# Optimization experiments

Measured on AMD Instinct MI355X. Metric: run time of the kernel, lower is better.

The kernel has to match this reference:

```python
import jax, jax.numpy as jnp
import numpy as np

MARGIN = 1.0
EPS = 1e-12


def setup_inputs() -> dict:
    key = jax.random.key(0)
    k1, k2, k3 = jax.random.split(key, 3)
    inputs = jax.random.normal(k1, (8192, 128), dtype=jnp.float32)
    targets = jax.random.randint(k2, (8192,), 0, 64, dtype=jnp.int64)
    center = jax.random.normal(k3, (16, 128), dtype=jnp.float32)
    return {"inputs": inputs, "targets": targets, "center": center}


def reference(inputs, targets, center):
    n = inputs.shape[0]
    # pairwise Euclidean distances via ||a||^2 + ||b||^2 - 2 a.b  (matches addmm_ trick)
    sq = jnp.sum(inputs * inputs, axis=1)                      # [n]
    dist2 = sq[:, None] + sq[None, :] - 2.0 * (inputs @ inputs.T)
    dist = jnp.sqrt(jnp.clip(dist2, EPS))                      # [n, n]

    mask = targets[:, None] == targets[None, :]                # same-class mask [n, n]

    # batch-hard mining, fully vectorized (replaces per-row python loops)
    dist_ap = jnp.max(jnp.where(mask, dist, -jnp.inf), axis=1)  # hardest positive
    neg_min = jnp.min(jnp.where(mask, jnp.inf, dist), axis=1)   # hardest negative
    has_neg = jnp.any(~mask, axis=1)
    dist_an = jnp.where(has_neg, neg_min, dist_ap + MARGIN)

    # center augmentation: min over distances to L2-normalized prototypes
    cn = center / jnp.linalg.norm(center, axis=1, keepdims=True)       # [P, d]
    dc = jnp.sqrt(jnp.sum((inputs[:, None, :] - cn[None, :, :]) ** 2, axis=-1))  # [n, P]
    dc = jnp.clip(dc, EPS)
    dist_an = jnp.minimum(dist_an, jnp.min(dc, axis=1))

    # MarginRankingLoss with y=1: mean(relu(dist_ap - dist_an + margin))
    loss = jnp.mean(jnp.maximum(dist_ap - dist_an + MARGIN, 0.0))
    return loss
```

## Files before the change

kernel.cpp:

```cpp
#include <hip/hip_runtime.h>


#define N_ROWS 8192
#define DIM 128
#define KDIM 192
#define ROWB 384
#define NPROTO 16
#define NSTRIP 16
#define MARGIN_F 1.0f
#define EPS_F 1e-12f
#define BIAS_F 32768.0f

typedef __attribute__((ext_vector_type(8))) short short8;
typedef __attribute__((ext_vector_type(4))) float float4v;
typedef __attribute__((ext_vector_type(4))) unsigned uint4v;

static __device__ __forceinline__ unsigned f2bf(float f) {
  unsigned u = __float_as_uint(f);
  u += 0x7fffu + ((u >> 16) & 1u);
  return u >> 16;
}

static __device__ __forceinline__ void gload_lds16(const void* g, void* l) {
  __builtin_amdgcn_global_load_lds(
      (const __attribute__((address_space(1))) unsigned*)g,
      (__attribute__((address_space(3))) unsigned*)l, 16, 0, 0);
}

__global__ void prep_kernel(const float* __restrict__ x,
                            const float* __restrict__ center,
                            const int* __restrict__ tgt,
                            char* __restrict__ xbf,
                            float* __restrict__ sq,
                            float* __restrict__ mindc,
                            float* __restrict__ out) {
  __shared__ float scn[NPROTO * DIM];
  int tid = threadIdx.x;
  if (blockIdx.x == 0 && tid == 0) out[0] = 0.0f;
  int rloc = tid >> 4, l = tid & 15;
  {
    float v[8];
    float ss = 0.f;
#pragma unroll
    for (int j = 0; j < 8; ++j) {
      v[j] = center[rloc * DIM + l * 8 + j];
      ss += v[j] * v[j];
    }
#pragma unroll
    for (int m = 1; m < 16; m <<= 1) ss += __shfl_xor(ss, m, 64);
    float inv = 1.0f / sqrtf(ss);
#pragma unroll
    for (int j = 0; j < 8; ++j) scn[rloc * DIM + l * 8 + j] = v[j] * inv;
  }
  __syncthreads();

  int row = blockIdx.x * 16 + rloc;
  float4 v0 = ((const float4*)x)[row * 32 + l * 2];
  float4 v1 = ((const float4*)x)[row * 32 + l * 2 + 1];
  float ss = v0.x * v0.x + v0.y * v0.y + v0.z * v0.z + v0.w * v0.w +
             v1.x * v1.x + v1.y * v1.y + v1.z * v1.z + v1.w * v1.w;
  float dots[NPROTO];
#pragma unroll
  for (int p = 0; p < NPROTO; ++p) {
    const float* c = &scn[p * DIM + l * 8];
    dots[p] = v0.x * c[0] + v0.y * c[1] + v0.z * c[2] + v0.w * c[3] +
              v1.x * c[4] + v1.y * c[5] + v1.z * c[6] + v1.w * c[7];
  }
#pragma unroll
  for (int m = 1; m < 16; m <<= 1) {
    ss += __shfl_xor(ss, m, 64);
#pragma unroll
    for (int p = 0; p < NPROTO; ++p) dots[p] += __shfl_xor(dots[p], m, 64);
  }
  uint4 pk;
  pk.x = f2bf(v0.x) | (f2bf(v0.y) << 16);
  pk.y = f2bf(v0.z) | (f2bf(v0.w) << 16);
  pk.z = f2bf(v1.x) | (f2bf(v1.y) << 16);
  pk.w = f2bf(v1.z) | (f2bf(v1.w) << 16);
  *(uint4*)(xbf + (size_t)row * ROWB + l * 16) = pk;
  int cls = tgt[row];
  if (l < 8) {
    unsigned wv = (cls & 1) ? 0xC3000000u : 0x0000C300u;
    uint4 oh;
    oh.x = ((cls >> 1) == (l * 4 + 0)) ? wv : 0u;
    oh.y = ((cls >> 1) == (l * 4 + 1)) ? wv : 0u;
    oh.z = ((cls >> 1) == (l * 4 + 2)) ? wv : 0u;
    oh.w = ((cls >> 1) == (l * 4 + 3)) ? wv : 0u;
    *(uint4*)(xbf + (size_t)row * ROWB + 256 + l * 16) = oh;
  }
  if (l == 0) {
    float mind2 = INFINITY;
#pragma unroll
    for (int p = 0; p < NPROTO; ++p)
      mind2 = fminf(mind2, ss + 1.0f - 2.0f * dots[p]);
    sq[row] = ss;
    mindc[row] = fmaxf(sqrtf(fmaxf(mind2, 0.0f)), EPS_F);
  }
}

__global__ __launch_bounds__(256, 1) void
pairdist_kernel(const char* __restrict__ xbf, const float* __restrict__ sq,
                float* __restrict__ pmax, float* __restrict__ pmin) {
  __shared__ __align__(16) char bl[3][24576];
  __shared__ __align__(16) float sqlds[512];
  const int wave = threadIdx.x >> 6, lane = threadIdx.x & 63;
  const int q = lane >> 4, l16 = lane & 15;
  const int rg = blockIdx.x >> 4, strip = blockIdx.x & 15;
  const int rowbase = rg * 256 + wave * 64;
  const int stripbase = strip * 512;

  const int slot = threadIdx.x;
  const char* const srcstrip = xbf + (size_t)stripbase * ROWB;
  int soff[6];
#pragma unroll
  for (int r = 0; r < 6; ++r) {
    int o = r * 4096 + slot * 16;
    int c = o / ROWB;
    soff[r] = c * ROWB + ((o - c * ROWB) ^ ((c & 7) << 4));
  }

  auto stage = [&](int s, char* buf) {
    const char* g = srcstrip + (size_t)s * 24576;
#pragma unroll
    for (int r = 0; r < 6; ++r)
      gload_lds16(g + soff[r], buf + r * 4096 + wave * 1024);
  };

  short8 a[4][6];
#pragma unroll
  for (int rt = 0; rt < 4; ++rt) {
    const char* ar = xbf + (size_t)(rowbase + rt * 16 + l16) * ROWB + q * 16;
#pragma unroll
    for (int kc = 0; kc < 6; ++kc) a[rt][kc] = *(const short8*)(ar + kc * 64);
#pragma unroll
    for (int kc = 4; kc < 6; ++kc) {
      uint4v u = __builtin_bit_cast(uint4v, a[rt][kc]);
      u ^= 0x80008000u;
      a[rt][kc] = __builtin_bit_cast(short8, u);
    }
  }
#pragma unroll
  for (int rt = 0; rt < 4; ++rt)
#pragma unroll
    for (int kc = 0; kc < 6; ++kc)
      asm volatile("" : "+v"(a[rt][kc]));

  if (wave < 2)
    gload_lds16((const char*)(sq + stripbase) + wave * 1024 + lane * 16,
                (char*)sqlds + wave * 1024 + lane * 16);
  stage(0, bl[0]);
  stage(1, bl[1]);

  int roffb[6];
#pragma unroll
  for (int kc = 0; kc < 6; ++kc)
    roffb[kc] = (l16 * ROWB + kc * 64 + q * 16) ^ ((l16 & 7) << 4);

  float maxp[16], minn[16];
#pragma unroll
  for (int i = 0; i < 16; ++i) { maxp[i] = -INFINITY; minn[i] = INFINITY; }

  asm volatile("s_waitcnt vmcnt(6)" ::: "memory");
  __builtin_amdgcn_s_barrier();
  asm volatile("" ::: "memory");

#pragma unroll 1
  for (int s = 0; s < 8; ++s) {
    if (s + 2 < 8) stage(s + 2, bl[(s + 2) % 3]);
    const char* cur = bl[s % 3];
#pragma unroll
    for (int p = 0; p < 4; ++p) {
      const char* bufp = cur + p * 6144;
      float sqc = sqlds[s * 64 + p * 16 + l16];
      short8 b[6];
#pragma unroll
      for (int kc = 0; kc < 6; ++kc)
        b[kc] = *(const short8*)(bufp + roffb[kc]);
      float4v acc[4];
#pragma unroll
      for (int rt = 0; rt < 4; ++rt) acc[rt] = (float4v){0.f, 0.f, 0.f, 0.f};
      __builtin_amdgcn_s_setprio(1);
#pragma unroll
      for (int kc = 0; kc < 6; ++kc)
#pragma unroll
        for (int rt = 0; rt < 4; ++rt)
          acc[rt] = __builtin_amdgcn_mfma_f32_16x16x32_bf16(a[rt][kc], b[kc],
                                                            acc[rt], 0, 0, 0);
      __builtin_amdgcn_s_setprio(0);
#pragma unroll
      for (int rt = 0; rt < 4; ++rt)
#pragma unroll
        for (int r = 0; r < 4; ++r) {
          float v = fmaf(-2.0f, acc[rt][r], sqc);
          int idx = rt * 4 + r;
          maxp[idx] = fmaxf(maxp[idx], v);
          minn[idx] = fminf(minn[idx], v);
        }
    }
    if (s < 7) {
      if (s + 2 < 8)
        asm volatile("s_waitcnt vmcnt(6)" ::: "memory");
      else
        asm volatile("s_waitcnt vmcnt(0)" ::: "memory");
      __builtin_amdgcn_s_barrier();
      asm volatile("" ::: "memory");
    }
  }

#pragma unroll
  for (int m = 1; m < 16; m <<= 1)
#pragma unroll
    for (int i = 0; i < 16; ++i) {
      maxp[i] = fmaxf(maxp[i], __shfl_xor(maxp[i], m, 64));
      minn[i] = fminf(minn[i], __shfl_xor(minn[i], m, 64));
    }
  if (l16 == 0) {
    float* pM = pmax + (size_t)strip * N_ROWS + rowbase + q * 4;
    float* pm = pmin + (size_t)strip * N_ROWS + rowbase + q * 4;
#pragma unroll
    for (int rt = 0; rt < 4; ++rt)
#pragma unroll
      for (int r = 0; r < 4; ++r) {
        pM[rt * 16 + r] = maxp[rt * 4 + r];
        pm[rt * 16 + r] = minn[rt * 4 + r];
      }
  }
}

__global__ void finalize_kernel(const float* __restrict__ pmax,
                                const float* __restrict__ pmin,
                                const float* __restrict__ sq,
                                const float* __restrict__ mindc,
                                float* __restrict__ out) {
  __shared__ float wsum[4];
  int i = blockIdx.x * 256 + threadIdx.x;
  float maxv = -INFINITY, minv = INFINITY;
#pragma unroll
  for (int s = 0; s < NSTRIP; ++s) {
    maxv = fmaxf(maxv, pmax[s * N_ROWS + i]);
    minv = fminf(minv, pmin[s * N_ROWS + i]);
  }
  float si = sq[i];
  float dap = sqrtf(fmaxf(si + (maxv - BIAS_F), EPS_F));
  float dan = (minv > 16384.0f) ? (dap + MARGIN_F)
                                : sqrtf(fmaxf(si + minv, EPS_F));
  dan = fminf(dan, mindc[i]);
  float c = fmaxf(dap - dan + MARGIN_F, 0.0f) * (1.0f / (float)N_ROWS);
#pragma unroll
  for (int m = 1; m < 64; m <<= 1) c += __shfl_xor(c, m, 64);
  int lane = threadIdx.x & 63, wv = threadIdx.x >> 6;
  if (lane == 0) wsum[wv] = c;
  __syncthreads();
  if (threadIdx.x == 0) atomicAdd(out, wsum[0] + wsum[1] + wsum[2] + wsum[3]);
}

extern "C" void kernel_launch(void* const* d_in, const int* in_sizes, int n_in,
                              void* d_out, int out_size, void* d_ws, size_t ws_size,
                              hipStream_t stream) {
  const float* inputs = (const float*)d_in[0];
  const int* targets = (const int*)d_in[1];
  const float* center = (const float*)d_in[2];
  char* ws = (char*)d_ws;
  char* xbf    = ws;
  float* sq    = (float*)(ws + 3145728);
  float* mindc = (float*)(ws + 3178496);
  float* pmax  = (float*)(ws + 3211264);
  float* pmin  = (float*)(ws + 3735552);
  float* out   = (float*)d_out;

  prep_kernel<<<512, 256, 0, stream>>>(inputs, center, targets, xbf, sq, mindc, out);
  pairdist_kernel<<<512, 256, 0, stream>>>(xbf, sq, pmax, pmin);
  finalize_kernel<<<32, 256, 0, stream>>>(pmax, pmin, sq, mindc, out);
}
```

Baseline: 104.6 us.

## Replace one-hot class bias in GEMM K-dim with explicit target-compare masking

The earlier version encoded class membership as extra one-hot K columns (K=192) with a large bias, so the MFMA produced a biased distance that separated positives from negatives. This change drops those columns, reducing K to 128, row bytes to 256, and LDS staging per stage. Same-class masking is now done per element by comparing targets, which are loaded into registers and LDS. It cuts MFMA work and memory traffic by a third and pays for it with extra compares and selects in the epilogue.

```diff
diff --git a/kernel.cpp b/kernel.cpp
--- a/kernel.cpp
+++ b/kernel.cpp
@@ -3,17 +3,14 @@
 
 #define N_ROWS 8192
 #define DIM 128
-#define KDIM 192
-#define ROWB 384
+#define ROWB 256
 #define NPROTO 16
 #define NSTRIP 16
 #define MARGIN_F 1.0f
 #define EPS_F 1e-12f
-#define BIAS_F 32768.0f
 
 typedef __attribute__((ext_vector_type(8))) short short8;
 typedef __attribute__((ext_vector_type(4))) float float4v;
-typedef __attribute__((ext_vector_type(4))) unsigned uint4v;
 
 static __device__ __forceinline__ unsigned f2bf(float f) {
   unsigned u = __float_as_uint(f);
@@ -29,7 +26,6 @@
 
 __global__ void prep_kernel(const float* __restrict__ x,
                             const float* __restrict__ center,
-                            const int* __restrict__ tgt,
                             char* __restrict__ xbf,
                             float* __restrict__ sq,
                             float* __restrict__ mindc,
@@ -78,16 +74,6 @@
   pk.z = f2bf(v1.x) | (f2bf(v1.y) << 16);
   pk.w = f2bf(v1.z) | (f2bf(v1.w) << 16);
   *(uint4*)(xbf + (size_t)row * ROWB + l * 16) = pk;
-  int cls = tgt[row];
-  if (l < 8) {
-    unsigned wv = (cls & 1) ? 0xC3000000u : 0x0000C300u;
-    uint4 oh;
-    oh.x = ((cls >> 1) == (l * 4 + 0)) ? wv : 0u;
-    oh.y = ((cls >> 1) == (l * 4 + 1)) ? wv : 0u;
-    oh.z = ((cls >> 1) == (l * 4 + 2)) ? wv : 0u;
-    oh.w = ((cls >> 1) == (l * 4 + 3)) ? wv : 0u;
-    *(uint4*)(xbf + (size_t)row * ROWB + 256 + l * 16) = oh;
-  }
   if (l == 0) {
     float mind2 = INFINITY;
 #pragma unroll
@@ -100,9 +86,11 @@
 
 __global__ __launch_bounds__(256, 1) void
 pairdist_kernel(const char* __restrict__ xbf, const float* __restrict__ sq,
+                const int* __restrict__ tgt,
                 float* __restrict__ pmax, float* __restrict__ pmin) {
-  __shared__ __align__(16) char bl[3][24576];
+  __shared__ __align__(16) char bl[3][16384];
   __shared__ __align__(16) float sqlds[512];
+  __shared__ __align__(16) int tgtlds[512];
   const int wave = threadIdx.x >> 6, lane = threadIdx.x & 63;
   const int q = lane >> 4, l16 = lane & 15;
   const int rg = blockIdx.x >> 4, strip = blockIdx.x & 15;
@@ -111,56 +99,64 @@
 
   const int slot = threadIdx.x;
   const char* const srcstrip = xbf + (size_t)stripbase * ROWB;
-  int soff[6];
-#pragma unroll
-  for (int r = 0; r < 6; ++r) {
+  int soff[4];
+#pragma unroll
+  for (int r = 0; r < 4; ++r) {
     int o = r * 4096 + slot * 16;
-    int c = o / ROWB;
-    soff[r] = c * ROWB + ((o - c * ROWB) ^ ((c & 7) << 4));
+    int c = o >> 8;
+    soff[r] = c * ROWB + ((o & 255) ^ ((c & 7) << 4));
   }
 
   auto stage = [&](int s, char* buf) {
-    const char* g = srcstrip + (size_t)s * 24576;
-#pragma unroll
-    for (int r = 0; r < 6; ++r)
+    const char* g = srcstrip + (size_t)s * 16384;
+#pragma unroll
+    for (int r = 0; r < 4; ++r)
       gload_lds16(g + soff[r], buf + r * 4096 + wave * 1024);
   };
 
-  short8 a[4][6];
+  short8 a[4][4];
 #pragma unroll
   for (int rt = 0; rt < 4; ++rt) {
     const char* ar = xbf + (size_t)(rowbase + rt * 16 + l16) * ROWB + q * 16;
 #pragma unroll
-    for (int kc = 0; kc < 6; ++kc) a[rt][kc] = *(const short8*)(ar + kc * 64);
-#pragma unroll
-    for (int kc = 4; kc < 6; ++kc) {
-      uint4v u = __builtin_bit_cast(uint4v, a[rt][kc]);
-      u ^= 0x80008000u;
-      a[rt][kc] = __builtin_bit_cast(short8, u);
-    }
-  }
-#pragma unroll
-  for (int rt = 0; rt < 4; ++rt)
-#pragma unroll
-    for (int kc = 0; kc < 6; ++kc)
+    for (int kc = 0; kc < 4; ++kc) a[rt][kc] = *(const short8*)(ar + kc * 64);
+  }
+  int trow[4][4];
+#pragma unroll
+  for (int rt = 0; rt < 4; ++rt) {
+    int4 t4 = ((const int4*)tgt)[(rowbase >> 2) + rt * 4 + q];
+    trow[rt][0] = t4.x; trow[rt][1] = t4.y;
+    trow[rt][2] = t4.z; trow[rt][3] = t4.w;
+  }
+#pragma unroll
+  for (int rt = 0; rt < 4; ++rt) {
+#pragma unroll
+    for (int kc = 0; kc < 4; ++kc)
       asm volatile("" : "+v"(a[rt][kc]));
+#pragma unroll
+    for (int r = 0; r < 4; ++r)
+      asm volatile("" : "+v"(trow[rt][r]));
+  }
 
   if (wave < 2)
     gload_lds16((const char*)(sq + stripbase) + wave * 1024 + lane * 16,
                 (char*)sqlds + wave * 1024 + lane * 16);
+  else
+    gload_lds16((const char*)(tgt + stripbase) + (wave - 2) * 1024 + lane * 16,
+                (char*)tgtlds + (wave - 2) * 1024 + lane * 16);
   stage(0, bl[0]);
   stage(1, bl[1]);
 
-  int roffb[6];
-#pragma unroll
-  for (int kc = 0; kc < 6; ++kc)
+  int roffb[4];
+#pragma unroll
+  for (int kc = 0; kc < 4; ++kc)
     roffb[kc] = (l16 * ROWB + kc * 64 + q * 16) ^ ((l16 & 7) << 4);
 
   float maxp[16], minn[16];
 #pragma unroll
   for (int i = 0; i < 16; ++i) { maxp[i] = -INFINITY; minn[i] = INFINITY; }
 
-  asm volatile("s_waitcnt vmcnt(6)" ::: "memory");
+  asm volatile("s_waitcnt vmcnt(4)" ::: "memory");
   __builtin_amdgcn_s_barrier();
   asm volatile("" ::: "memory");
 
@@ -170,18 +166,19 @@
     const char* cur = bl[s % 3];
 #pragma unroll
     for (int p = 0; p < 4; ++p) {
-      const char* bufp = cur + p * 6144;
+      const char* bufp = cur + p * 4096;
       float sqc = sqlds[s * 64 + p * 16 + l16];
-      short8 b[6];
-#pragma unroll
-      for (int kc = 0; kc < 6; ++kc)
+      int tcc = tgtlds[s * 64 + p * 16 + l16];
+      short8 b[4];
+#pragma unroll
+      for (int kc = 0; kc < 4; ++kc)
         b[kc] = *(const short8*)(bufp + roffb[kc]);
       float4v acc[4];
 #pragma unroll
       for (int rt = 0; rt < 4; ++rt) acc[rt] = (float4v){0.f, 0.f, 0.f, 0.f};
       __builtin_amdgcn_s_setprio(1);
 #pragma unroll
-      for (int kc = 0; kc < 6; ++kc)
+      for (int kc = 0; kc < 4; ++kc)
 #pragma unroll
         for (int rt = 0; rt < 4; ++rt)
           acc[rt] = __builtin_amdgcn_mfma_f32_16x16x32_bf16(a[rt][kc], b[kc],
@@ -192,14 +189,15 @@
 #pragma unroll
         for (int r = 0; r < 4; ++r) {
           float v = fmaf(-2.0f, acc[rt][r], sqc);
+          bool sm = (tcc == trow[rt][r]);
           int idx = rt * 4 + r;
-          maxp[idx] = fmaxf(maxp[idx], v);
-          minn[idx] = fminf(minn[idx], v);
+          maxp[idx] = sm ? fmaxf(maxp[idx], v) : maxp[idx];
+          minn[idx] = sm ? minn[idx] : fminf(minn[idx], v);
         }
     }
     if (s < 7) {
       if (s + 2 < 8)
-        asm volatile("s_waitcnt vmcnt(6)" ::: "memory");
+        asm volatile("s_waitcnt vmcnt(4)" ::: "memory");
       else
         asm volatile("s_waitcnt vmcnt(0)" ::: "memory");
       __builtin_amdgcn_s_barrier();
@@ -241,9 +239,8 @@
     minv = fminf(minv, pmin[s * N_ROWS + i]);
   }
   float si = sq[i];
-  float dap = sqrtf(fmaxf(si + (maxv - BIAS_F), EPS_F));
-  float dan = (minv > 16384.0f) ? (dap + MARGIN_F)
-                                : sqrtf(fmaxf(si + minv, EPS_F));
+  float dap = sqrtf(fmaxf(si + maxv, EPS_F));
+  float dan = (minv > 1e37f) ? (dap + MARGIN_F) : sqrtf(fmaxf(si + minv, EPS_F));
   dan = fminf(dan, mindc[i]);
   float c = fmaxf(dap - dan + MARGIN_F, 0.0f) * (1.0f / (float)N_ROWS);
 #pragma unroll
@@ -262,13 +259,13 @@
   const float* center = (const float*)d_in[2];
   char* ws = (char*)d_ws;
   char* xbf    = ws;
-  float* sq    = (float*)(ws + 3145728);
-  float* mindc = (float*)(ws + 3178496);
-  float* pmax  = (float*)(ws + 3211264);
-  float* pmin  = (float*)(ws + 3735552);
+  float* sq    = (float*)(ws + 2097152);
+  float* mindc = (float*)(ws + 2129920);
+  float* pmax  = (float*)(ws + 2162688);
+  float* pmin  = (float*)(ws + 2686976);
   float* out   = (float*)d_out;
 
-  prep_kernel<<<512, 256, 0, stream>>>(inputs, center, targets, xbf, sq, mindc, out);
-  pairdist_kernel<<<512, 256, 0, stream>>>(xbf, sq, pmax, pmin);
+  prep_kernel<<<512, 256, 0, stream>>>(inputs, center, xbf, sq, mindc, out);
+  pairdist_kernel<<<512, 256, 0, stream>>>(xbf, sq, targets, pmax, pmin);
   finalize_kernel<<<32, 256, 0, stream>>>(pmax, pmin, sq, mindc, out);
 }
```

Result: faster. 101.5 us (-3.0%).
